# Kernel optimization log

Hardware: AMD Instinct MI355X
Metric: run time of the kernel (lower is better)

The kernel has to match this reference:

```python
import jax, jax.numpy as jnp
import numpy as np

NUM_HEADS = 8

def setup_inputs() -> dict:
    key = jax.random.key(0)
    k1, k2, k3, k4, k5 = jax.random.split(key, 5)
    B, N, C = 4, 2048, 512
    x = jax.random.normal(k1, (B, N, C), dtype=jnp.float32)
    s = 1.0 / np.sqrt(C)
    qkv_w = jax.random.uniform(k2, (3 * C, C), dtype=jnp.float32, minval=-s, maxval=s)
    qkv_b = jax.random.uniform(k3, (3 * C,), dtype=jnp.float32, minval=-s, maxval=s)
    proj_w = jax.random.uniform(k4, (C, C), dtype=jnp.float32, minval=-s, maxval=s)
    proj_b = jax.random.uniform(k5, (C,), dtype=jnp.float32, minval=-s, maxval=s)
    return {"x": x, "qkv_w": qkv_w, "qkv_b": qkv_b, "proj_w": proj_w, "proj_b": proj_b}

def reference(x, qkv_w, qkv_b, proj_w, proj_b):
    B, N, C = x.shape
    H = NUM_HEADS
    D = C // H
    scale = D ** -0.5
    # qkv: [B,N,3C] -> [3,B,H,N,D]
    qkv = (jnp.einsum('bnc,oc->bno', x, qkv_w) + qkv_b)
    qkv = qkv.reshape(B, N, 3, H, D).transpose(2, 0, 3, 1, 4)
    q, k, v = qkv[0], qkv[1], qkv[2]
    attn = jnp.einsum('bhnd,bhmd->bhnm', q, k) * scale  # [B,H,N,N]
    attn = jax.nn.softmax(attn, axis=-1)
    out = jnp.einsum('bhnm,bhmd->bhnd', attn, v)  # [B,H,N,D]
    out = out.transpose(0, 2, 1, 3).reshape(B, N, C)
    return jnp.einsum('bnc,oc->bno', out, proj_w) + proj_b
```

## Files before the change

### kernel.cpp

```cpp
#include <hip/hip_runtime.h>
#include <stdint.h>


typedef short bf16x8 __attribute__((ext_vector_type(8)));
typedef float f32x2  __attribute__((ext_vector_type(2)));
typedef float f32x4  __attribute__((ext_vector_type(4)));
typedef float f32x16 __attribute__((ext_vector_type(16)));
typedef unsigned int u32x4 __attribute__((ext_vector_type(4)));

__device__ __forceinline__ unsigned short f2bf(float f) {
    unsigned int u = __builtin_bit_cast(unsigned int, f);
    u += 0x7fffu + ((u >> 16) & 1u);
    return (unsigned short)(u >> 16);
}
__device__ __forceinline__ unsigned int pk2(float a, float b) {
    return (unsigned int)f2bf(a) | ((unsigned int)f2bf(b) << 16);
}
__device__ __forceinline__ float fexp2(float x) {
    return __builtin_amdgcn_exp2f(x);
}
__device__ __forceinline__ bf16x8 ld8_f32(const float* __restrict__ p) {
    float4 f0 = *(const float4*)p;
    float4 f1 = *(const float4*)(p + 4);
    u32x4 u = {pk2(f0.x, f0.y), pk2(f0.z, f0.w), pk2(f1.x, f1.y), pk2(f1.z, f1.w)};
    return __builtin_bit_cast(bf16x8, u);
}
__device__ __forceinline__ void async16(const void* g, void* l) {
    __builtin_amdgcn_global_load_lds(
        (const __attribute__((address_space(1))) unsigned int*)g,
        (__attribute__((address_space(3))) unsigned int*)l,
        16, 0, 0);
}

#define MFMA16(a, b, c) __builtin_amdgcn_mfma_f32_16x16x32_bf16((a), (b), (c), 0, 0, 0)
#define MFMA32(a, b, c) __builtin_amdgcn_mfma_f32_32x32x16_bf16((a), (b), (c), 0, 0, 0)

__global__ void cvt_bf16(const float* __restrict__ x,
                         const float* __restrict__ w,
                         const float* __restrict__ w2,
                         unsigned short* __restrict__ xb,
                         unsigned short* __restrict__ wb,
                         unsigned short* __restrict__ wb2)
{
    const int G = 524288 + 98304 + 32768;
    for (int idx = blockIdx.x * 256 + threadIdx.x; idx < G; idx += gridDim.x * 256) {
        if (idx < 524288)
            *(bf16x8*)(xb + (size_t)idx * 8) = ld8_f32(x + (size_t)idx * 8);
        else if (idx < 524288 + 98304) {
            int j = idx - 524288;
            *(bf16x8*)(wb + (size_t)j * 8) = ld8_f32(w + (size_t)j * 8);
        } else {
            int j = idx - 524288 - 98304;
            *(bf16x8*)(wb2 + (size_t)j * 8) = ld8_f32(w2 + (size_t)j * 8);
        }
    }
}

__global__ __launch_bounds__(256, 4)
void gemm_qkv(const unsigned short* __restrict__ A,
              const unsigned short* __restrict__ B,
              const float* __restrict__ bias,
              unsigned short* __restrict__ out0,
              unsigned short* __restrict__ out1,
              unsigned short* __restrict__ out2,
              int K)
{
    __shared__ unsigned short sA[128 * 32];
    __shared__ unsigned short sB[128 * 32];

    const int tid  = threadIdx.x;
    const int wave = tid >> 6, lane = tid & 63;
    const int l = lane & 15, q16 = lane >> 4;
    const int wm = wave >> 1, wn = wave & 1;
    const int bid = blockIdx.x;
    const int slot = bid >> 3;
    const int m0 = ((bid & 7) * 8 + slot / 12) * 128;
    const int n0 = (slot % 12) * 128;

    f32x4 acc[4][4];
#pragma unroll
    for (int i = 0; i < 4; ++i)
#pragma unroll
        for (int j = 0; j < 4; ++j)
            acc[i][j] = (f32x4){0.f, 0.f, 0.f, 0.f};

    for (int k0 = 0; k0 < K; k0 += 32) {
#pragma unroll
        for (int call = 0; call < 2; ++call) {
            int L = call * 256 + tid;
            int r = L >> 2, c = L & 3;
            async16(A + (size_t)(m0 + r) * K + k0 + c * 8, sA + L * 8);
            async16(B + (size_t)(n0 + r) * K + k0 + c * 8, sB + L * 8);
        }
        __syncthreads();

        bf16x8 af[4], bfr[4];
#pragma unroll
        for (int i = 0; i < 4; ++i)
            af[i] = *(const bf16x8*)(sA + ((wm * 64 + i * 16 + l) * 4 + q16) * 8);
#pragma unroll
        for (int j = 0; j < 4; ++j)
            bfr[j] = *(const bf16x8*)(sB + ((wn * 64 + j * 16 + l) * 4 + q16) * 8);
#pragma unroll
        for (int i = 0; i < 4; ++i)
#pragma unroll
            for (int j = 0; j < 4; ++j)
                acc[i][j] = MFMA16(af[i], bfr[j], acc[i][j]);
        __syncthreads();
    }

    const float lscale = 0.18033688f;
#pragma unroll
    for (int i = 0; i < 4; ++i) {
#pragma unroll
        for (int j = 0; j < 4; ++j) {
            int col = n0 + wn * 64 + j * 16 + l;
            float bv = bias[col];
#pragma unroll
            for (int r = 0; r < 4; ++r) {
                int row = m0 + wm * 64 + i * 16 + q16 * 4 + r;
                float val = acc[i][j][r] + bv;
                int which = col >> 9;
                int h = (col >> 6) & 7, d = col & 63;
                int b = row >> 11, n = row & 2047;
                if (which == 0)
                    out0[(size_t)(((b * 8 + h) * 2048) + n) * 64 + d] = f2bf(val * lscale);
                else if (which == 1)
                    out1[(size_t)(((b * 8 + h) * 2048) + n) * 64 + d] = f2bf(val);
                else {
                    int np = (n & ~12) | ((n & 8) >> 1) | ((n & 4) << 1);
                    out2[(size_t)(((b * 8 + h) * 64) + d) * 2048 + np] = f2bf(val);
                }
            }
        }
    }
}

__global__ __launch_bounds__(256, 4)
void gemm_out(const unsigned short* __restrict__ A,
              const unsigned short* __restrict__ B,
              const float* __restrict__ bias,
              float* __restrict__ outf,
              int K, int N)
{
    __shared__ unsigned short sA[64 * 32];
    __shared__ unsigned short sB[128 * 32];

    const int tid  = threadIdx.x;
    const int wave = tid >> 6, lane = tid & 63;
    const int l = lane & 15, q16 = lane >> 4;
    const int wm = wave >> 1, wn = wave & 1;
    const int bid = blockIdx.x;
    const int slot = bid >> 3;
    const int m0 = ((bid & 7) * 16 + (slot >> 2)) * 64;
    const int n0 = (slot & 3) * 128;

    f32x4 acc[2][4];
#pragma unroll
    for (int i = 0; i < 2; ++i)
#pragma unroll
        for (int j = 0; j < 4; ++j)
            acc[i][j] = (f32x4){0.f, 0.f, 0.f, 0.f};

    for (int k0 = 0; k0 < K; k0 += 32) {
        {
            int r = tid >> 2, c = tid & 3;
            async16(A + (size_t)(m0 + r) * K + k0 + c * 8, sA + tid * 8);
        }
#pragma unroll
        for (int call = 0; call < 2; ++call) {
            int L = call * 256 + tid;
            int r = L >> 2, c = L & 3;
            async16(B + (size_t)(n0 + r) * K + k0 + c * 8, sB + L * 8);
        }
        __syncthreads();

        bf16x8 af[2], bfr[4];
#pragma unroll
        for (int i = 0; i < 2; ++i)
            af[i] = *(const bf16x8*)(sA + ((wm * 32 + i * 16 + l) * 4 + q16) * 8);
#pragma unroll
        for (int j = 0; j < 4; ++j)
            bfr[j] = *(const bf16x8*)(sB + ((wn * 64 + j * 16 + l) * 4 + q16) * 8);
#pragma unroll
        for (int i = 0; i < 2; ++i)
#pragma unroll
            for (int j = 0; j < 4; ++j)
                acc[i][j] = MFMA16(af[i], bfr[j], acc[i][j]);
        __syncthreads();
    }

#pragma unroll
    for (int i = 0; i < 2; ++i) {
#pragma unroll
        for (int j = 0; j < 4; ++j) {
            int col = n0 + wn * 64 + j * 16 + l;
            float bv = bias[col];
#pragma unroll
            for (int r = 0; r < 4; ++r) {
                int row = m0 + wm * 32 + i * 16 + q16 * 4 + r;
                outf[(size_t)row * N + col] = acc[i][j][r] + bv;
            }
        }
    }
}

__global__ __launch_bounds__(512)
void attn_fused(const unsigned short* __restrict__ Q,
                const unsigned short* __restrict__ Km,
                const unsigned short* __restrict__ Vt,
                unsigned short* __restrict__ O)
{
    __shared__ unsigned short sAll[49152];

    const int tid  = threadIdx.x;
    const int wave = tid >> 6, lane = tid & 63;
    const int l31 = lane & 31, h = lane >> 5;
    const int swz = l31 & 7;
    const int qq = wave & 3, kh = wave >> 2;
    const int bid = blockIdx.x;
    const int slot = bid >> 3;
    const int bh = (bid & 7) * 4 + (slot >> 3);
    const int qc = slot & 7;
    const int q0 = qc * 256 + qq * 64;

    const unsigned short* Kp = Km + (size_t)bh * 2048 * 64;
    const unsigned short* Vp = Vt + (size_t)bh * 64 * 2048;
    unsigned short* sKf = sAll;
    unsigned short* sVf = sAll + 24576;

    int ka[4], va[2][2];
#pragma unroll
    for (int ks = 0; ks < 4; ++ks)
        ka[ks] = (kh * 64 + l31) * 64 + ((ks * 2 + h) ^ swz) * 8;
#pragma unroll
    for (int m1 = 0; m1 < 2; ++m1)
#pragma unroll
        for (int ks2 = 0; ks2 < 2; ++ks2)
            va[m1][ks2] = l31 * 128 + ((m1 * 4 + ks2 * 2 + h) ^ swz) * 8 + kh * 64;

    int ksrc[2], vsrc[2], dsl[2];
#pragma unroll
    for (int c = 0; c < 2; ++c) {
        int s = c * 512 + tid;
        int rk = s >> 3;
        ksrc[c] = rk * 64 + ((s & 7) ^ (rk & 7)) * 8;
        int rv = s >> 4;
        vsrc[c] = rv * 2048 + ((s & 15) ^ (rv & 7)) * 8;
        dsl[c] = s * 8;
    }

    bf16x8 qf[2][4];
#pragma unroll
    for (int qt = 0; qt < 2; ++qt)
#pragma unroll
        for (int ks = 0; ks < 4; ++ks)
            qf[qt][ks] = *(const bf16x8*)(Q + (size_t)(bh * 2048 + q0 + qt * 32 + l31) * 64
                                          + ks * 16 + h * 8);

    f32x16 oacc[2][2];
#pragma unroll
    for (int qt = 0; qt < 2; ++qt)
#pragma unroll
        for (int dt = 0; dt < 2; ++dt)
#pragma unroll
            for (int e = 0; e < 16; ++e) oacc[qt][dt][e] = 0.f;
    f32x16 Zv;
#pragma unroll
    for (int e = 0; e < 16; ++e) Zv[e] = 0.f;
    f32x2 l2[2];
    l2[0] = (f32x2){0.f, 0.f};
    l2[1] = (f32x2){0.f, 0.f};

    f32x16 sA0, sA1, sB0, sB1;
    bf16x8 vfpA = __builtin_bit_cast(bf16x8, (u32x4){0u, 0u, 0u, 0u});
    bf16x8 vfpB = vfpA, vfpC = vfpA, vfpD = vfpA;

    auto qk = [&](const unsigned short* sKc, int mtOff, f32x16& d0, f32x16& d1) {
        bf16x8 kf = *(const bf16x8*)(sKc + ka[0] + mtOff);
        __builtin_amdgcn_s_setprio(1);
        d0 = MFMA32(kf, qf[0][0], Zv);
        d1 = MFMA32(kf, qf[1][0], Zv);
        __builtin_amdgcn_s_setprio(0);
#pragma unroll
        for (int ks = 1; ks < 4; ++ks) {
            kf = *(const bf16x8*)(sKc + ka[ks] + mtOff);
            __builtin_amdgcn_s_setprio(1);
            d0 = MFMA32(kf, qf[0][ks], d0);
            d1 = MFMA32(kf, qf[1][ks], d1);
            __builtin_amdgcn_s_setprio(0);
        }
    };

    auto softmax_pack = [&](const f32x16& s0, const f32x16& s1,
                            bf16x8& f00, bf16x8& f01,
                            bf16x8& f10, bf16x8& f11) {
        unsigned int pk0[4][2], pk1[4][2];
#pragma unroll
        for (int g = 0; g < 4; ++g) {
            float a0 = fexp2(s0[4 * g + 0]);
            float a1 = fexp2(s0[4 * g + 1]);
            float a2 = fexp2(s0[4 * g + 2]);
            float a3 = fexp2(s0[4 * g + 3]);
            l2[0] += (f32x2){a0, a1};
            l2[0] += (f32x2){a2, a3};
            pk0[g][0] = __builtin_amdgcn_perm(
                __builtin_bit_cast(unsigned int, a1),
                __builtin_bit_cast(unsigned int, a0), 0x07060302u);
            pk0[g][1] = __builtin_amdgcn_perm(
                __builtin_bit_cast(unsigned int, a3),
                __builtin_bit_cast(unsigned int, a2), 0x07060302u);
            float b0 = fexp2(s1[4 * g + 0]);
            float b1 = fexp2(s1[4 * g + 1]);
            float b2 = fexp2(s1[4 * g + 2]);
            float b3 = fexp2(s1[4 * g + 3]);
            l2[1] += (f32x2){b0, b1};
            l2[1] += (f32x2){b2, b3};
            pk1[g][0] = __builtin_amdgcn_perm(
                __builtin_bit_cast(unsigned int, b1),
                __builtin_bit_cast(unsigned int, b0), 0x07060302u);
            pk1[g][1] = __builtin_amdgcn_perm(
                __builtin_bit_cast(unsigned int, b3),
                __builtin_bit_cast(unsigned int, b2), 0x07060302u);
        }
        u32x4 bu;
        bu[0] = pk0[0][0]; bu[1] = pk0[0][1]; bu[2] = pk0[1][0]; bu[3] = pk0[1][1];
        f00 = __builtin_bit_cast(bf16x8, bu);
        bu[0] = pk0[2][0]; bu[1] = pk0[2][1]; bu[2] = pk0[3][0]; bu[3] = pk0[3][1];
        f01 = __builtin_bit_cast(bf16x8, bu);
        bu[0] = pk1[0][0]; bu[1] = pk1[0][1]; bu[2] = pk1[1][0]; bu[3] = pk1[1][1];
        f10 = __builtin_bit_cast(bf16x8, bu);
        bu[0] = pk1[2][0]; bu[1] = pk1[2][1]; bu[2] = pk1[3][0]; bu[3] = pk1[3][1];
        f11 = __builtin_bit_cast(bf16x8, bu);
    };

    auto pv_lds = [&](bf16x8 f00, bf16x8 f01, bf16x8 f10, bf16x8 f11,
                      int mt, const unsigned short* sVc) {
        bf16x8 v00 = *(const bf16x8*)(sVc + va[mt][0]);
        bf16x8 v01 = *(const bf16x8*)(sVc + va[mt][0] + 4096);
        bf16x8 v10 = *(const bf16x8*)(sVc + va[mt][1]);
        bf16x8 v11 = *(const bf16x8*)(sVc + va[mt][1] + 4096);
        __builtin_amdgcn_s_setprio(1);
        oacc[0][0] = MFMA32(v00, f00, oacc[0][0]);
        oacc[1][0] = MFMA32(v00, f10, oacc[1][0]);
        oacc[0][1] = MFMA32(v01, f00, oacc[0][1]);
        oacc[1][1] = MFMA32(v01, f10, oacc[1][1]);
        oacc[0][0] = MFMA32(v10, f01, oacc[0][0]);
        oacc[1][0] = MFMA32(v10, f11, oacc[1][0]);
        oacc[0][1] = MFMA32(v11, f01, oacc[0][1]);
        oacc[1][1] = MFMA32(v11, f11, oacc[1][1]);
        __builtin_amdgcn_s_setprio(0);
    };

    auto pv_reg = [&](bf16x8 f00, bf16x8 f01, bf16x8 f10, bf16x8 f11) {
        __builtin_amdgcn_s_setprio(1);
        oacc[0][0] = MFMA32(vfpA, f00, oacc[0][0]);
        oacc[1][0] = MFMA32(vfpA, f10, oacc[1][0]);
        oacc[0][1] = MFMA32(vfpB, f00, oacc[0][1]);
        oacc[1][1] = MFMA32(vfpB, f10, oacc[1][1]);
        oacc[0][0] = MFMA32(vfpC, f01, oacc[0][0]);
        oacc[1][0] = MFMA32(vfpC, f11, oacc[1][0]);
        oacc[0][1] = MFMA32(vfpD, f01, oacc[0][1]);
        oacc[1][1] = MFMA32(vfpD, f11, oacc[1][1]);
        __builtin_amdgcn_s_setprio(0);
    };

#pragma unroll
    for (int c = 0; c < 2; ++c) {
        async16(Kp + ksrc[c], (void*)(sKf + dsl[c]));
        async16(Vp + vsrc[c], (void*)(sVf + dsl[c]));
    }
#pragma unroll
    for (int c = 0; c < 2; ++c) {
        async16(Kp + (size_t)128 * 64 + ksrc[c], (void*)(sKf + 8192 + dsl[c]));
        async16(Vp + (size_t)128 + vsrc[c], (void*)(sVf + 8192 + dsl[c]));
    }
    asm volatile("s_waitcnt vmcnt(4)" ::: "memory");
    __builtin_amdgcn_s_barrier();
    __builtin_amdgcn_sched_barrier(0);

    int off0 = 0, off1 = 8192, off2 = 16384;

    for (int t = 0; t < 16; ++t) {
        const unsigned short* sKc = sKf + off0;
        const unsigned short* sVc = sVf + off0;

        if (t < 14) {
            size_t kv = (size_t)(t + 2) * 128;
#pragma unroll
            for (int c = 0; c < 2; ++c) {
                async16(Kp + kv * 64 + ksrc[c], (void*)(sKf + off2 + dsl[c]));
                async16(Vp + kv + vsrc[c], (void*)(sVf + off2 + dsl[c]));
            }
        }

        if (kh == 1 && t > 0) {
            bf16x8 f00, f01, f10, f11;
            softmax_pack(sB0, sB1, f00, f01, f10, f11);
            pv_reg(f00, f01, f10, f11);
        }

        qk(sKc, 0, sA0, sA1);
        {
            bf16x8 f00, f01, f10, f11;
            softmax_pack(sA0, sA1, f00, f01, f10, f11);
            pv_lds(f00, f01, f10, f11, 0, sVc);
        }

        if (kh == 0) {
            qk(sKc, 2048, sB0, sB1);
            bf16x8 f00, f01, f10, f11;
            softmax_pack(sB0, sB1, f00, f01, f10, f11);
            pv_lds(f00, f01, f10, f11, 1, sVc);
        } else {
            qk(sKc, 2048, sB0, sB1);
            vfpA = *(const bf16x8*)(sVc + va[1][0]);
            vfpB = *(const bf16x8*)(sVc + va[1][0] + 4096);
            vfpC = *(const bf16x8*)(sVc + va[1][1]);
            vfpD = *(const bf16x8*)(sVc + va[1][1] + 4096);
        }

        if (t < 14) {
            asm volatile("s_waitcnt vmcnt(4)" ::: "memory");
        } else if (t == 14) {
            asm volatile("s_waitcnt vmcnt(0)" ::: "memory");
        }
        if (t < 15) {
            asm volatile("s_waitcnt lgkmcnt(0)" ::: "memory");
            __builtin_amdgcn_s_barrier();
            __builtin_amdgcn_sched_barrier(0);
        }
        int tmp = off0; off0 = off1; off1 = off2; off2 = tmp;
    }

    if (kh == 1) {
        bf16x8 f00, f01, f10, f11;
        softmax_pack(sB0, sB1, f00, f01, f10, f11);
        pv_reg(f00, f01, f10, f11);
    }

    __syncthreads();
    float* sf = (float*)sAll;
    float* sl = sf + 16384;
    if (kh == 1) {
        const int base = (qq * 64 + lane) * 64;
#pragma unroll
        for (int qt = 0; qt < 2; ++qt)
#pragma unroll
            for (int dt = 0; dt < 2; ++dt) {
                int chunk = (qt * 2 + dt) ^ (lane & 3);
                *(f32x16*)(sf + base + chunk * 16) = oacc[qt][dt];
            }
        *(f32x2*)(sl + (qq * 64 + lane) * 4 + 0) = l2[0];
        *(f32x2*)(sl + (qq * 64 + lane) * 4 + 2) = l2[1];
    }
    __syncthreads();
    if (kh == 0) {
        const int base = (qq * 64 + lane) * 64;
#pragma unroll
        for (int qt = 0; qt < 2; ++qt)
#pragma unroll
            for (int dt = 0; dt < 2; ++dt) {
                int chunk = (qt * 2 + dt) ^ (lane & 3);
                f32x16 part = *(const f32x16*)(sf + base + chunk * 16);
#pragma unroll
                for (int e = 0; e < 16; ++e) oacc[qt][dt][e] += part[e];
            }
        l2[0] += *(const f32x2*)(sl + (qq * 64 + lane) * 4 + 0);
        l2[1] += *(const f32x2*)(sl + (qq * 64 + lane) * 4 + 2);

        const int b = bh >> 3, hh = bh & 7;
#pragma unroll
        for (int qt = 0; qt < 2; ++qt) {
            float l_run = l2[qt][0] + l2[qt][1];
            l_run += __shfl_xor(l_run, 32);
            float inv = 1.f / fmaxf(l_run, 1e-20f);
            unsigned short* obase = O + ((size_t)(b * 2048 + q0 + qt * 32 + l31)) * 512 + hh * 64;
#pragma unroll
            for (int dt = 0; dt < 2; ++dt)
#pragma unroll
                for (int g = 0; g < 4; ++g) {
                    int d = dt * 32 + 8 * g + 4 * h;
                    unsigned int w0 = pk2(oacc[qt][dt][4 * g + 0] * inv,
                                          oacc[qt][dt][4 * g + 1] * inv);
                    unsigned int w1 = pk2(oacc[qt][dt][4 * g + 2] * inv,
                                          oacc[qt][dt][4 * g + 3] * inv);
                    uint2 w = {w0, w1};
                    *(uint2*)(obase + d) = w;
                }
        }
    }
}

extern "C" void kernel_launch(void* const* d_in, const int* in_sizes, int n_in,
                              void* d_out, int out_size, void* d_ws, size_t ws_size,
                              hipStream_t stream)
{
    const float* x      = (const float*)d_in[0];
    const float* qkv_w  = (const float*)d_in[1];
    const float* qkv_b  = (const float*)d_in[2];
    const float* proj_w = (const float*)d_in[3];
    const float* proj_b = (const float*)d_in[4];

    const size_t PER = 4u * 8u * 2048u * 64u;
    unsigned short* q_ws  = (unsigned short*)d_ws;
    unsigned short* k_ws  = q_ws  + PER;
    unsigned short* vt_ws = k_ws  + PER;
    unsigned short* ao_ws = vt_ws + PER;
    unsigned short* wb2   = ao_ws + PER;

    unsigned short* xb = (unsigned short*)d_out;
    unsigned short* wb = xb + PER;

    cvt_bf16<<<dim3(640), 256, 0, stream>>>(x, qkv_w, proj_w, xb, wb, wb2);
    gemm_qkv<<<dim3(768), 256, 0, stream>>>(xb, wb, qkv_b, q_ws, k_ws, vt_ws, 512);
    attn_fused<<<dim3(256), 512, 0, stream>>>(q_ws, k_ws, vt_ws, ao_ws);
    gemm_out<<<dim3(512), 256, 0, stream>>>(ao_ws, wb2, proj_b, (float*)d_out, 512, 512);
}
```

Before: 155.4 us.

## Store K/V in MFMA fragment layout and load directly from global, dropping LDS staging

The QKV GEMM epilogue now writes K and V in a pre-swizzled, per-lane MFMA fragment order. The attention kernel can then load each operand fragment with one contiguous 16-byte global load per lane instead of staging tiles through shared memory with async copies and barriers. This removes the LDS pipeline, the barriers and the waitcnt choreography, and shrinks shared memory to what the final merge needs. The cost is that K/V tiles are re-read from global/L2 by every wave that uses them, and load latency is hidden only by register double-buffering.

```diff
diff --git a/kernel.cpp b/kernel.cpp
--- a/kernel.cpp
+++ b/kernel.cpp
@@ -121,15 +121,26 @@
                 int row = m0 + wm * 64 + i * 16 + q16 * 4 + r;
                 float val = acc[i][j][r] + bv;
                 int which = col >> 9;
-                int h = (col >> 6) & 7, d = col & 63;
+                int hd = (col >> 6) & 7, d = col & 63;
                 int b = row >> 11, n = row & 2047;
-                if (which == 0)
-                    out0[(size_t)(((b * 8 + h) * 2048) + n) * 64 + d] = f2bf(val * lscale);
-                else if (which == 1)
-                    out1[(size_t)(((b * 8 + h) * 2048) + n) * 64 + d] = f2bf(val);
-                else {
+                int bh = b * 8 + hd;
+                if (which == 0) {
+                    out0[(size_t)((bh * 2048) + n) * 64 + d] = f2bf(val * lscale);
+                } else if (which == 1) {
+                    int t = n >> 7, kh2 = (n >> 6) & 1, mt = (n >> 5) & 1;
+                    int l31o = n & 31;
+                    int ks = (d >> 4) & 3, h2 = (d >> 3) & 1, e = d & 7;
+                    size_t frag = ((((size_t)bh * 16 + t) * 2 + kh2) * 2 + mt) * 4 + ks;
+                    out1[frag * 512 + (h2 * 32 + l31o) * 8 + e] = f2bf(val);
+                } else {
                     int np = (n & ~12) | ((n & 8) >> 1) | ((n & 4) << 1);
-                    out2[(size_t)(((b * 8 + h) * 64) + d) * 2048 + np] = f2bf(val);
+                    int t = np >> 7, kh2 = (np >> 6) & 1;
+                    int c = (np >> 3) & 7, e = np & 7;
+                    int m1 = (c >> 2) & 1, ks2 = (c >> 1) & 1, h2 = c & 1;
+                    int dt = d >> 5, l31o = d & 31;
+                    size_t frag = (((((size_t)bh * 16 + t) * 2 + kh2) * 2 + m1) * 2
+                                   + ks2) * 2 + dt;
+                    out2[frag * 512 + (h2 * 32 + l31o) * 8 + e] = f2bf(val);
                 }
             }
         }
@@ -207,16 +218,15 @@
 
 __global__ __launch_bounds__(512)
 void attn_fused(const unsigned short* __restrict__ Q,
-                const unsigned short* __restrict__ Km,
-                const unsigned short* __restrict__ Vt,
+                const unsigned short* __restrict__ Kfr,
+                const unsigned short* __restrict__ Vfr,
                 unsigned short* __restrict__ O)
 {
-    __shared__ unsigned short sAll[49152];
+    __shared__ float smrg[16384 + 1024];
 
     const int tid  = threadIdx.x;
     const int wave = tid >> 6, lane = tid & 63;
     const int l31 = lane & 31, h = lane >> 5;
-    const int swz = l31 & 7;
     const int qq = wave & 3, kh = wave >> 2;
     const int bid = blockIdx.x;
     const int slot = bid >> 3;
@@ -224,31 +234,8 @@
     const int qc = slot & 7;
     const int q0 = qc * 256 + qq * 64;
 
-    const unsigned short* Kp = Km + (size_t)bh * 2048 * 64;
-    const unsigned short* Vp = Vt + (size_t)bh * 64 * 2048;
-    unsigned short* sKf = sAll;
-    unsigned short* sVf = sAll + 24576;
-
-    int ka[4], va[2][2];
-#pragma unroll
-    for (int ks = 0; ks < 4; ++ks)
-        ka[ks] = (kh * 64 + l31) * 64 + ((ks * 2 + h) ^ swz) * 8;
-#pragma unroll
-    for (int m1 = 0; m1 < 2; ++m1)
-#pragma unroll
-        for (int ks2 = 0; ks2 < 2; ++ks2)
-            va[m1][ks2] = l31 * 128 + ((m1 * 4 + ks2 * 2 + h) ^ swz) * 8 + kh * 64;
-
-    int ksrc[2], vsrc[2], dsl[2];
-#pragma unroll
-    for (int c = 0; c < 2; ++c) {
-        int s = c * 512 + tid;
-        int rk = s >> 3;
-        ksrc[c] = rk * 64 + ((s & 7) ^ (rk & 7)) * 8;
-        int rv = s >> 4;
-        vsrc[c] = rv * 2048 + ((s & 15) ^ (rv & 7)) * 8;
-        dsl[c] = s * 8;
-    }
+    const unsigned short* Kb = Kfr + (size_t)bh * 131072 + kh * 4096 + lane * 8;
+    const unsigned short* Vb = Vfr + (size_t)bh * 131072 + kh * 4096 + lane * 8;
 
     bf16x8 qf[2][4];
 #pragma unroll
@@ -271,26 +258,6 @@
     f32x2 l2[2];
     l2[0] = (f32x2){0.f, 0.f};
     l2[1] = (f32x2){0.f, 0.f};
-
-    f32x16 sA0, sA1, sB0, sB1;
-    bf16x8 vfpA = __builtin_bit_cast(bf16x8, (u32x4){0u, 0u, 0u, 0u});
-    bf16x8 vfpB = vfpA, vfpC = vfpA, vfpD = vfpA;
-
-    auto qk = [&](const unsigned short* sKc, int mtOff, f32x16& d0, f32x16& d1) {
-        bf16x8 kf = *(const bf16x8*)(sKc + ka[0] + mtOff);
-        __builtin_amdgcn_s_setprio(1);
-        d0 = MFMA32(kf, qf[0][0], Zv);
-        d1 = MFMA32(kf, qf[1][0], Zv);
-        __builtin_amdgcn_s_setprio(0);
-#pragma unroll
-        for (int ks = 1; ks < 4; ++ks) {
-            kf = *(const bf16x8*)(sKc + ka[ks] + mtOff);
-            __builtin_amdgcn_s_setprio(1);
-            d0 = MFMA32(kf, qf[0][ks], d0);
-            d1 = MFMA32(kf, qf[1][ks], d1);
-            __builtin_amdgcn_s_setprio(0);
-        }
-    };
 
     auto softmax_pack = [&](const f32x16& s0, const f32x16& s1,
                             bf16x8& f00, bf16x8& f01,
@@ -334,114 +301,88 @@
         f11 = __builtin_bit_cast(bf16x8, bu);
     };
 
-    auto pv_lds = [&](bf16x8 f00, bf16x8 f01, bf16x8 f10, bf16x8 f11,
-                      int mt, const unsigned short* sVc) {
-        bf16x8 v00 = *(const bf16x8*)(sVc + va[mt][0]);
-        bf16x8 v01 = *(const bf16x8*)(sVc + va[mt][0] + 4096);
-        bf16x8 v10 = *(const bf16x8*)(sVc + va[mt][1]);
-        bf16x8 v11 = *(const bf16x8*)(sVc + va[mt][1] + 4096);
+    bf16x8 kA[4], kB[4], vv[2][2];
+
+#pragma unroll
+    for (int ks = 0; ks < 4; ++ks)
+        kA[ks] = *(const bf16x8*)(Kb + ks * 512);
+
+    for (int t = 0; t < 16; ++t) {
+        const size_t tb = (size_t)t * 8192;
+
+#pragma unroll
+        for (int ks2 = 0; ks2 < 2; ++ks2)
+#pragma unroll
+            for (int dt = 0; dt < 2; ++dt)
+                vv[ks2][dt] = *(const bf16x8*)(Vb + tb + ks2 * 1024 + dt * 512);
+#pragma unroll
+        for (int ks = 0; ks < 4; ++ks)
+            kB[ks] = *(const bf16x8*)(Kb + tb + 2048 + ks * 512);
+
+        f32x16 s0, s1;
         __builtin_amdgcn_s_setprio(1);
-        oacc[0][0] = MFMA32(v00, f00, oacc[0][0]);
-        oacc[1][0] = MFMA32(v00, f10, oacc[1][0]);
-        oacc[0][1] = MFMA32(v01, f00, oacc[0][1]);
-        oacc[1][1] = MFMA32(v01, f10, oacc[1][1]);
-        oacc[0][0] = MFMA32(v10, f01, oacc[0][0]);
-        oacc[1][0] = MFMA32(v10, f11, oacc[1][0]);
-        oacc[0][1] = MFMA32(v11, f01, oacc[0][1]);
-        oacc[1][1] = MFMA32(v11, f11, oacc[1][1]);
+        s0 = MFMA32(kA[0], qf[0][0], Zv);
+        s1 = MFMA32(kA[0], qf[1][0], Zv);
+#pragma unroll
+        for (int ks = 1; ks < 4; ++ks) {
+            s0 = MFMA32(kA[ks], qf[0][ks], s0);
+            s1 = MFMA32(kA[ks], qf[1][ks], s1);
+        }
         __builtin_amdgcn_s_setprio(0);
-    };
-
-    auto pv_reg = [&](bf16x8 f00, bf16x8 f01, bf16x8 f10, bf16x8 f11) {
-        __builtin_amdgcn_s_setprio(1);
-        oacc[0][0] = MFMA32(vfpA, f00, oacc[0][0]);
-        oacc[1][0] = MFMA32(vfpA, f10, oacc[1][0]);
-        oacc[0][1] = MFMA32(vfpB, f00, oacc[0][1]);
-        oacc[1][1] = MFMA32(vfpB, f10, oacc[1][1]);
-        oacc[0][0] = MFMA32(vfpC, f01, oacc[0][0]);
-        oacc[1][0] = MFMA32(vfpC, f11, oacc[1][0]);
-        oacc[0][1] = MFMA32(vfpD, f01, oacc[0][1]);
-        oacc[1][1] = MFMA32(vfpD, f11, oacc[1][1]);
-        __builtin_amdgcn_s_setprio(0);
-    };
-
-#pragma unroll
-    for (int c = 0; c < 2; ++c) {
-        async16(Kp + ksrc[c], (void*)(sKf + dsl[c]));
-        async16(Vp + vsrc[c], (void*)(sVf + dsl[c]));
-    }
-#pragma unroll
-    for (int c = 0; c < 2; ++c) {
-        async16(Kp + (size_t)128 * 64 + ksrc[c], (void*)(sKf + 8192 + dsl[c]));
-        async16(Vp + (size_t)128 + vsrc[c], (void*)(sVf + 8192 + dsl[c]));
-    }
-    asm volatile("s_waitcnt vmcnt(4)" ::: "memory");
-    __builtin_amdgcn_s_barrier();
-    __builtin_amdgcn_sched_barrier(0);
-
-    int off0 = 0, off1 = 8192, off2 = 16384;
-
-    for (int t = 0; t < 16; ++t) {
-        const unsigned short* sKc = sKf + off0;
-        const unsigned short* sVc = sVf + off0;
-
-        if (t < 14) {
-            size_t kv = (size_t)(t + 2) * 128;
-#pragma unroll
-            for (int c = 0; c < 2; ++c) {
-                async16(Kp + kv * 64 + ksrc[c], (void*)(sKf + off2 + dsl[c]));
-                async16(Vp + kv + vsrc[c], (void*)(sVf + off2 + dsl[c]));
-            }
-        }
-
-        if (kh == 1 && t > 0) {
-            bf16x8 f00, f01, f10, f11;
-            softmax_pack(sB0, sB1, f00, f01, f10, f11);
-            pv_reg(f00, f01, f10, f11);
-        }
-
-        qk(sKc, 0, sA0, sA1);
         {
             bf16x8 f00, f01, f10, f11;
-            softmax_pack(sA0, sA1, f00, f01, f10, f11);
-            pv_lds(f00, f01, f10, f11, 0, sVc);
-        }
-
-        if (kh == 0) {
-            qk(sKc, 2048, sB0, sB1);
+            softmax_pack(s0, s1, f00, f01, f10, f11);
+            __builtin_amdgcn_s_setprio(1);
+            oacc[0][0] = MFMA32(vv[0][0], f00, oacc[0][0]);
+            oacc[1][0] = MFMA32(vv[0][0], f10, oacc[1][0]);
+            oacc[0][1] = MFMA32(vv[0][1], f00, oacc[0][1]);
+            oacc[1][1] = MFMA32(vv[0][1], f10, oacc[1][1]);
+            oacc[0][0] = MFMA32(vv[1][0], f01, oacc[0][0]);
+            oacc[1][0] = MFMA32(vv[1][0], f11, oacc[1][0]);
+            oacc[0][1] = MFMA32(vv[1][1], f01, oacc[0][1]);
+            oacc[1][1] = MFMA32(vv[1][1], f11, oacc[1][1]);
+            __builtin_amdgcn_s_setprio(0);
+        }
+
+#pragma unroll
+        for (int ks2 = 0; ks2 < 2; ++ks2)
+#pragma unroll
+            for (int dt = 0; dt < 2; ++dt)
+                vv[ks2][dt] = *(const bf16x8*)(Vb + tb + 2048 + ks2 * 1024 + dt * 512);
+        if (t < 15) {
+#pragma unroll
+            for (int ks = 0; ks < 4; ++ks)
+                kA[ks] = *(const bf16x8*)(Kb + tb + 8192 + ks * 512);
+        }
+
+        __builtin_amdgcn_s_setprio(1);
+        s0 = MFMA32(kB[0], qf[0][0], Zv);
+        s1 = MFMA32(kB[0], qf[1][0], Zv);
+#pragma unroll
+        for (int ks = 1; ks < 4; ++ks) {
+            s0 = MFMA32(kB[ks], qf[0][ks], s0);
+            s1 = MFMA32(kB[ks], qf[1][ks], s1);
+        }
+        __builtin_amdgcn_s_setprio(0);
+        {
             bf16x8 f00, f01, f10, f11;
-            softmax_pack(sB0, sB1, f00, f01, f10, f11);
-            pv_lds(f00, f01, f10, f11, 1, sVc);
-        } else {
-            qk(sKc, 2048, sB0, sB1);
-            vfpA = *(const bf16x8*)(sVc + va[1][0]);
-            vfpB = *(const bf16x8*)(sVc + va[1][0] + 4096);
-            vfpC = *(const bf16x8*)(sVc + va[1][1]);
-            vfpD = *(const bf16x8*)(sVc + va[1][1] + 4096);
-        }
-
-        if (t < 14) {
-            asm volatile("s_waitcnt vmcnt(4)" ::: "memory");
-        } else if (t == 14) {
-            asm volatile("s_waitcnt vmcnt(0)" ::: "memory");
-        }
-        if (t < 15) {
-            asm volatile("s_waitcnt lgkmcnt(0)" ::: "memory");
-            __builtin_amdgcn_s_barrier();
-            __builtin_amdgcn_sched_barrier(0);
-        }
-        int tmp = off0; off0 = off1; off1 = off2; off2 = tmp;
-    }
-
-    if (kh == 1) {
-        bf16x8 f00, f01, f10, f11;
-        softmax_pack(sB0, sB1, f00, f01, f10, f11);
-        pv_reg(f00, f01, f10, f11);
+            softmax_pack(s0, s1, f00, f01, f10, f11);
+            __builtin_amdgcn_s_setprio(1);
+            oacc[0][0] = MFMA32(vv[0][0], f00, oacc[0][0]);
+            oacc[1][0] = MFMA32(vv[0][0], f10, oacc[1][0]);
+            oacc[0][1] = MFMA32(vv[0][1], f00, oacc[0][1]);
+            oacc[1][1] = MFMA32(vv[0][1], f10, oacc[1][1]);
+            oacc[0][0] = MFMA32(vv[1][0], f01, oacc[0][0]);
+            oacc[1][0] = MFMA32(vv[1][0], f11, oacc[1][0]);
+            oacc[0][1] = MFMA32(vv[1][1], f01, oacc[0][1]);
+            oacc[1][1] = MFMA32(vv[1][1], f11, oacc[1][1]);
+            __builtin_amdgcn_s_setprio(0);
+        }
     }
 
     __syncthreads();
-    float* sf = (float*)sAll;
-    float* sl = sf + 16384;
+    float* sf = smrg;
+    float* sl = smrg + 16384;
     if (kh == 1) {
         const int base = (qq * 64 + lane) * 64;
 #pragma unroll
```

After: 151.6 us, median of 2. -2.5%, faster.
